# Kernel optimization log

Measured on AMD Instinct MI355X. Metric: run time of the kernel, lower is better.

The kernel has to match this reference:

```python
import jax, jax.numpy as jnp
import numpy as np

B, IN, N, E = 2048, 1024, 64, 128
NEG_SLOPE = 0.01  # torch LeakyReLU default

def setup_inputs() -> dict:
    key = jax.random.key(0)
    k = jax.random.split(key, 5)
    scale_in = 1.0 / np.sqrt(IN)
    scale_ctx = 1.0 / np.sqrt(2 * E)
    return {
        "x": jax.random.normal(k[0], (B, IN), dtype=jnp.float32),
        # stacked per-concept Linear(in_features, 2*emb_size)
        "W_ctx": jax.random.uniform(k[1], (N, IN, 2 * E), jnp.float32, -scale_in, scale_in),
        "b_ctx": jax.random.uniform(k[2], (N, 2 * E), jnp.float32, -scale_in, scale_in),
        # shared Linear(2*emb_size, 1)
        "w_prob": jax.random.uniform(k[3], (2 * E,), jnp.float32, -scale_ctx, scale_ctx),
        "b_prob": jax.random.uniform(k[4], (), jnp.float32, -scale_ctx, scale_ctx),
    }

def reference(x, W_ctx, b_ctx, w_prob, b_prob):
    # context: [B, N, 2E] = LeakyReLU(x @ W_i + b_i) for all concepts i at once
    ctx = jnp.einsum("bi,nio->bno", x, W_ctx) + b_ctx
    ctx = jnp.where(ctx >= 0, ctx, NEG_SLOPE * ctx)
    # shared gate: [B, N]
    c_pred = jax.nn.sigmoid(jnp.einsum("bno,o->bn", ctx, w_prob) + b_prob)
    # gated blend of positive/negative halves -> [B, N, E]
    p = c_pred[..., None]
    c_emb = ctx[..., :E] * p + ctx[..., E:] * (1.0 - p)
    return c_emb, c_pred
```

## Files before the change

kernel.cpp:

```cpp
#include <hip/hip_runtime.h>
#include <hip/hip_bf16.h>

typedef __attribute__((ext_vector_type(8))) short short8v;
typedef __attribute__((ext_vector_type(4))) float floatx4;

#define B_ROWS 2048
#define K_DIM  1024
#define N_CON  64
#define TWO_E  256
#define E_DIM  128
#define BM     128
#define BK     64
#define NT     16
#define LDSA_BYTES (BM * BK * 2)
#define SMEM_BYTES (2 * LDSA_BYTES)
#define EMB_ELEMS 16777216ULL
#define WT_BYTES  33554432ULL
#define XB_BYTES  4194304ULL

static __device__ inline unsigned short bf16bits(float f) {
    __hip_bfloat16 h = __float2bfloat16(f);
    unsigned short u;
    __builtin_memcpy(&u, &h, 2);
    return u;
}

static __device__ inline void dma16(const void* g, void* l) {
    __builtin_amdgcn_global_load_lds(
        (const __attribute__((address_space(1))) unsigned int*)g,
        (__attribute__((address_space(3))) unsigned int*)l,
        16, 0, 0);
}

__global__ void __launch_bounds__(256) prep(const float* __restrict__ W,
                                            const float* __restrict__ x,
                                            unsigned short* __restrict__ Wt,
                                            unsigned short* __restrict__ xb) {
    __shared__ unsigned int lds2[64 * 36];
    const int tid = threadIdx.x;
    const int ot = blockIdx.x, ktile = blockIdx.y, n = blockIdx.z;
    const float* src = W + ((size_t)n * K_DIM + (size_t)ktile * 64) * TWO_E + ot * 64;
    unsigned short* dst = Wt + ((size_t)n * TWO_E + (size_t)ot * 64) * K_DIM + ktile * 64;

    const int kp = tid >> 4;
    const int c  = (tid & 15) * 4;
#pragma unroll
    for (int it = 0; it < 2; ++it) {
        const int k0 = it * 32 + kp * 2;
        floatx4 r0 = *(const floatx4*)&src[(size_t)k0 * TWO_E + c];
        floatx4 r1 = *(const floatx4*)&src[(size_t)(k0 + 1) * TWO_E + c];
#pragma unroll
        for (int j = 0; j < 4; ++j) {
            unsigned int d = (unsigned int)bf16bits(r0[j]) |
                             ((unsigned int)bf16bits(r1[j]) << 16);
            lds2[(c + j) * 36 + it * 16 + kp] = d;
        }
    }
    __syncthreads();
#pragma unroll
    for (int it = 0; it < 2; ++it) {
        int q = it * 256 + tid;
        int o = q >> 3, kc = q & 7;
        short8v v = *(short8v*)&lds2[o * 36 + kc * 4];
        *(short8v*)&dst[(size_t)o * K_DIM + kc * 8] = v;
    }

    const int bid = blockIdx.x + blockIdx.y * 4 + blockIdx.z * 64;
    const size_t base = (size_t)bid * 512 + (size_t)tid * 2;
    unsigned int d = (unsigned int)bf16bits(x[base]) |
                     ((unsigned int)bf16bits(x[base + 1]) << 16);
    ((unsigned int*)xb)[base >> 1] = d;
}

__global__ void __launch_bounds__(256, 2)
concept5(const unsigned short* __restrict__ xb,
         const unsigned short* __restrict__ Wt,
         const float* __restrict__ bc,
         const float* __restrict__ wp,
         const float* __restrict__ bp,
         float* __restrict__ out) {
    __shared__ __align__(16) char smem[SMEM_BYTES];

    const int tid  = threadIdx.x;
    const int wave = tid >> 6;
    const int lane = tid & 63;
    const int lg   = lane >> 4;
    const int l15  = lane & 15;
    const int og   = wave;

    const int lin = blockIdx.y * 16 + blockIdx.x;
    const int nid = (lin & 7) * 128 + (lin >> 3);
    const int rb  = nid & 15;
    const int n   = nid >> 4;

    int otile[4];
#pragma unroll
    for (int oi = 0; oi < 4; ++oi) otile[oi] = og * 32 + (oi & 1) * 16 + (oi & 2) * 64;

    floatx4 acc[8][4];
#pragma unroll
    for (int mi = 0; mi < 8; ++mi)
#pragma unroll
        for (int oi = 0; oi < 4; ++oi) acc[mi][oi] = (floatx4){0.f, 0.f, 0.f, 0.f};

    const unsigned short* xrow = xb + (size_t)rb * BM * K_DIM;
    const unsigned short* wb[4];
#pragma unroll
    for (int oi = 0; oi < 4; ++oi)
        wb[oi] = Wt + ((size_t)n * TWO_E + otile[oi] + l15) * K_DIM + lg * 8;

    const int sw0 = ((lg) ^ (l15 & 7)) * 16;
    const int sw1 = ((4 + lg) ^ (l15 & 7)) * 16;
    const int abase = l15 * 128;

#pragma unroll
    for (int it = 0; it < 4; ++it) {
        int c = it * 4 + wave;
        int s = c * 64 + lane;
        int r = s >> 3, g = s & 7;
        dma16(xrow + (size_t)r * K_DIM + ((g ^ (r & 7)) * 8), smem + c * 1024);
    }
    __syncthreads();

#pragma unroll 1
    for (int t = 0; t < NT; ++t) {
        const int kt = t * BK;
        char* ldsR = smem + (t & 1) * LDSA_BYTES;

        short8v bfr[4][2];
#pragma unroll
        for (int oi = 0; oi < 4; ++oi)
#pragma unroll
            for (int ks = 0; ks < 2; ++ks)
                bfr[oi][ks] = *(const short8v*)(wb[oi] + kt + ks * 32);

        if (t + 1 < NT) {
            char* ldsW = smem + ((t + 1) & 1) * LDSA_BYTES;
            const int ktn = kt + BK;
#pragma unroll
            for (int it = 0; it < 4; ++it) {
                int c = it * 4 + wave;
                int s = c * 64 + lane;
                int r = s >> 3, g = s & 7;
                dma16(xrow + (size_t)r * K_DIM + ktn + ((g ^ (r & 7)) * 8),
                      ldsW + c * 1024);
            }
        }

#pragma unroll
        for (int mi = 0; mi < 8; ++mi) {
            short8v a0 = *(const short8v*)(ldsR + abase + mi * 2048 + sw0);
            short8v a1 = *(const short8v*)(ldsR + abase + mi * 2048 + sw1);
#pragma unroll
            for (int oi = 0; oi < 4; ++oi) {
                acc[mi][oi] = __builtin_amdgcn_mfma_f32_16x16x32_bf16(
                    a0, bfr[oi][0], acc[mi][oi], 0, 0, 0);
                acc[mi][oi] = __builtin_amdgcn_mfma_f32_16x16x32_bf16(
                    a1, bfr[oi][1], acc[mi][oi], 0, 0, 0);
            }
        }

        __syncthreads();
    }

    float biasf[4], wpf[4];
#pragma unroll
    for (int oi = 0; oi < 4; ++oi) {
        int o = otile[oi] + l15;
        biasf[oi] = bc[n * TWO_E + o];
        wpf[oi]  = wp[o];
    }
#pragma unroll
    for (int mi = 0; mi < 8; ++mi)
#pragma unroll
        for (int oi = 0; oi < 4; ++oi)
#pragma unroll
            for (int j = 0; j < 4; ++j) {
                float v = acc[mi][oi][j] + biasf[oi];
                acc[mi][oi][j] = v >= 0.f ? v : 0.01f * v;
            }

    float* partial = (float*)smem;
    float* pv      = (float*)(smem + 2048);

#pragma unroll
    for (int mi = 0; mi < 8; ++mi)
#pragma unroll
        for (int j = 0; j < 4; ++j) {
            float ps = 0.f;
#pragma unroll
            for (int oi = 0; oi < 4; ++oi) ps += acc[mi][oi][j] * wpf[oi];
            ps += __shfl_xor(ps, 1);
            ps += __shfl_xor(ps, 2);
            ps += __shfl_xor(ps, 4);
            ps += __shfl_xor(ps, 8);
            if (l15 == 0) partial[(mi * 16 + lg * 4 + j) * 4 + og] = ps;
        }
    __syncthreads();

    if (tid < 128) {
        float s = partial[tid * 4] + partial[tid * 4 + 1] + partial[tid * 4 + 2] +
                  partial[tid * 4 + 3] + bp[0];
        float p = 1.f / (1.f + __expf(-s));
        pv[tid] = p;
        size_t bi = (size_t)rb * BM + tid;
        out[EMB_ELEMS + bi * N_CON + n] = p;
    }
    __syncthreads();

#pragma unroll
    for (int mi = 0; mi < 8; ++mi)
#pragma unroll
        for (int oi = 0; oi < 2; ++oi)
#pragma unroll
            for (int j = 0; j < 4; ++j) {
                int row = mi * 16 + lg * 4 + j;
                int e = og * 32 + oi * 16 + l15;
                float p = pv[row];
                float v = acc[mi][oi][j] * p + acc[mi][oi + 2][j] * (1.f - p);
                size_t bi = (size_t)rb * BM + row;
                out[(bi * N_CON + n) * E_DIM + e] = v;
            }
}

__global__ void __launch_bounds__(512, 4)
concept_fallback(const float* __restrict__ x,
                 const float* __restrict__ Wc,
                 const float* __restrict__ bc,
                 const float* __restrict__ wp,
                 const float* __restrict__ bp,
                 float* __restrict__ out) {
    __shared__ __align__(16) char smem[49152];
    char* ldsA = smem;
    char* ldsB = smem + 16384;

    const int tid  = threadIdx.x;
    const int wave = tid >> 6;
    const int lane = tid & 63;
    const int lg   = lane >> 4;
    const int l15  = lane & 15;
    const int h    = wave >> 2;
    const int og   = wave & 3;
    const int rb = blockIdx.x;
    const int n  = blockIdx.y;

    int otile[4];
#pragma unroll
    for (int oi = 0; oi < 4; ++oi) otile[oi] = og * 32 + (oi & 1) * 16 + (oi & 2) * 64;

    floatx4 acc[4][4];
#pragma unroll
    for (int mi = 0; mi < 4; ++mi)
#pragma unroll
        for (int oi = 0; oi < 4; ++oi) acc[mi][oi] = (floatx4){0.f, 0.f, 0.f, 0.f};

    const float* xg = x + (size_t)rb * BM * K_DIM;
    const float* wg = Wc + (size_t)n * K_DIM * TWO_E;

    for (int kt = 0; kt < K_DIM; kt += BK) {
#pragma unroll
        for (int it = 0; it < 2; ++it) {
            int s = it * 512 + tid;
            int r = s >> 3, g = s & 7;
            const float* p = xg + (size_t)r * K_DIM + kt + ((g ^ (r & 7)) * 8);
            floatx4 v0 = *(const floatx4*)p, v1 = *(const floatx4*)(p + 4);
            short8v b;
            b[0] = (short)bf16bits(v0[0]); b[1] = (short)bf16bits(v0[1]);
            b[2] = (short)bf16bits(v0[2]); b[3] = (short)bf16bits(v0[3]);
            b[4] = (short)bf16bits(v1[0]); b[5] = (short)bf16bits(v1[1]);
            b[6] = (short)bf16bits(v1[2]); b[7] = (short)bf16bits(v1[3]);
            *(short8v*)(ldsA + s * 16) = b;
        }
#pragma unroll
        for (int it = 0; it < 4; ++it) {
            int s = it * 512 + tid;
            int r = s >> 3, g = s & 7;
            int k0 = kt + (g ^ (r & 7)) * 8;
            short8v b;
#pragma unroll
            for (int j = 0; j < 8; ++j)
                b[j] = (short)bf16bits(wg[(size_t)(k0 + j) * TWO_E + r]);
            *(short8v*)(ldsB + s * 16) = b;
        }
        __syncthreads();

#pragma unroll
        for (int ks = 0; ks < 2; ++ks) {
            const int sw = ((ks * 4 + lg) ^ (l15 & 7)) * 16;
            short8v af[4], bfr[4];
#pragma unroll
            for (int mi = 0; mi < 4; ++mi)
                af[mi] = *(const short8v*)(ldsA + (h * 64 + mi * 16 + l15) * 128 + sw);
#pragma unroll
            for (int oi = 0; oi < 4; ++oi)
                bfr[oi] = *(const short8v*)(ldsB + (otile[oi] + l15) * 128 + sw);
#pragma unroll
            for (int mi = 0; mi < 4; ++mi)
#pragma unroll
                for (int oi = 0; oi < 4; ++oi)
                    acc[mi][oi] = __builtin_amdgcn_mfma_f32_16x16x32_bf16(
                        af[mi], bfr[oi], acc[mi][oi], 0, 0, 0);
        }
        __syncthreads();
    }

    float biasf[4], wpf[4];
#pragma unroll
    for (int oi = 0; oi < 4; ++oi) {
        int o = otile[oi] + l15;
        biasf[oi] = bc[n * TWO_E + o];
        wpf[oi]  = wp[o];
    }
#pragma unroll
    for (int mi = 0; mi < 4; ++mi)
#pragma unroll
        for (int oi = 0; oi < 4; ++oi)
#pragma unroll
            for (int j = 0; j < 4; ++j) {
                float v = acc[mi][oi][j] + biasf[oi];
                acc[mi][oi][j] = v >= 0.f ? v : 0.01f * v;
            }

    float* partial = (float*)smem;
    float* pv      = (float*)(smem + 2048);

#pragma unroll
    for (int mi = 0; mi < 4; ++mi)
#pragma unroll
        for (int j = 0; j < 4; ++j) {
            float ps = 0.f;
#pragma unroll
            for (int oi = 0; oi < 4; ++oi) ps += acc[mi][oi][j] * wpf[oi];
            ps += __shfl_xor(ps, 1);
            ps += __shfl_xor(ps, 2);
            ps += __shfl_xor(ps, 4);
            ps += __shfl_xor(ps, 8);
            if (l15 == 0) partial[(h * 64 + mi * 16 + lg * 4 + j) * 4 + og] = ps;
        }
    __syncthreads();

    if (tid < 128) {
        float s = partial[tid * 4] + partial[tid * 4 + 1] + partial[tid * 4 + 2] +
                  partial[tid * 4 + 3] + bp[0];
        float p = 1.f / (1.f + __expf(-s));
        pv[tid] = p;
        size_t bi = (size_t)rb * BM + tid;
        out[EMB_ELEMS + bi * N_CON + n] = p;
    }
    __syncthreads();

#pragma unroll
    for (int mi = 0; mi < 4; ++mi)
#pragma unroll
        for (int oi = 0; oi < 2; ++oi)
#pragma unroll
            for (int j = 0; j < 4; ++j) {
                int row = h * 64 + mi * 16 + lg * 4 + j;
                int e = og * 32 + oi * 16 + l15;
                float p = pv[row];
                float v = acc[mi][oi][j] * p + acc[mi][oi + 2][j] * (1.f - p);
                size_t bi = (size_t)rb * BM + row;
                out[(bi * N_CON + n) * E_DIM + e] = v;
            }
}

extern "C" void kernel_launch(void* const* d_in, const int* in_sizes, int n_in,
                              void* d_out, int out_size, void* d_ws, size_t ws_size,
                              hipStream_t stream) {
    const float* x  = (const float*)d_in[0];
    const float* Wc = (const float*)d_in[1];
    const float* bc = (const float*)d_in[2];
    const float* wp = (const float*)d_in[3];
    const float* bp = (const float*)d_in[4];
    float* out = (float*)d_out;

    if (ws_size >= WT_BYTES + XB_BYTES) {
        unsigned short* Wt = (unsigned short*)d_ws;
        unsigned short* xb = (unsigned short*)((char*)d_ws + WT_BYTES);
        prep<<<dim3(4, 16, 64), 256, 0, stream>>>(Wc, x, Wt, xb);
        concept5<<<dim3(16, 64), 256, 0, stream>>>(xb, Wt, bc, wp, bp, out);
    } else {
        concept_fallback<<<dim3(16, 64), 512, 0, stream>>>(
            x, Wc, bc, wp, bp, out);
    }
}
```

Before: 212.4 us.

## Prefetch weight fragments one K-tile ahead and shrink prep LDS padding

The main GEMM loop now loads the next K-tile's weight fragments from global memory into a second register buffer while the current tile's MFMAs run. The loop is unrolled by two so the two buffers swap roles without copies, which hides global load latency behind compute. The cost is more live vector registers under a 2-blocks-per-SM launch bound, so spilling is possible. Separately, the prep transpose's LDS row stride drops from 36 to 33 words to change bank mapping, which leaves the 16-byte LDS reads unaligned on odd rows.

```diff
diff --git a/kernel.cpp b/kernel.cpp
--- a/kernel.cpp
+++ b/kernel.cpp
@@ -36,7 +36,7 @@
                                             const float* __restrict__ x,
                                             unsigned short* __restrict__ Wt,
                                             unsigned short* __restrict__ xb) {
-    __shared__ unsigned int lds2[64 * 36];
+    __shared__ unsigned int lds2[64 * 33];
     const int tid = threadIdx.x;
     const int ot = blockIdx.x, ktile = blockIdx.y, n = blockIdx.z;
     const float* src = W + ((size_t)n * K_DIM + (size_t)ktile * 64) * TWO_E + ot * 64;
@@ -53,7 +53,7 @@
         for (int j = 0; j < 4; ++j) {
             unsigned int d = (unsigned int)bf16bits(r0[j]) |
                              ((unsigned int)bf16bits(r1[j]) << 16);
-            lds2[(c + j) * 36 + it * 16 + kp] = d;
+            lds2[(c + j) * 33 + it * 16 + kp] = d;
         }
     }
     __syncthreads();
@@ -61,7 +61,7 @@
     for (int it = 0; it < 2; ++it) {
         int q = it * 256 + tid;
         int o = q >> 3, kc = q & 7;
-        short8v v = *(short8v*)&lds2[o * 36 + kc * 4];
+        short8v v = *(short8v*)&lds2[o * 33 + kc * 4];
         *(short8v*)&dst[(size_t)o * K_DIM + kc * 8] = v;
     }
 
@@ -73,7 +73,7 @@
 }
 
 __global__ void __launch_bounds__(256, 2)
-concept5(const unsigned short* __restrict__ xb,
+concept6(const unsigned short* __restrict__ xb,
          const unsigned short* __restrict__ Wt,
          const float* __restrict__ bc,
          const float* __restrict__ wp,
@@ -120,48 +120,56 @@
         int r = s >> 3, g = s & 7;
         dma16(xrow + (size_t)r * K_DIM + ((g ^ (r & 7)) * 8), smem + c * 1024);
     }
-    __syncthreads();
+    short8v bA[4][2], bB[4][2];
+#pragma unroll
+    for (int oi = 0; oi < 4; ++oi)
+#pragma unroll
+        for (int ks = 0; ks < 2; ++ks)
+            bA[oi][ks] = *(const short8v*)(wb[oi] + ks * 32);
+    __syncthreads();
+
+#define TILE_BODY(T, CUR, NXT)                                                \
+    {                                                                         \
+        const int t_ = (T);                                                   \
+        if (t_ + 1 < NT) {                                                    \
+            const int ktn = (t_ + 1) * BK;                                    \
+            _Pragma("unroll")                                                 \
+            for (int oi = 0; oi < 4; ++oi) {                                  \
+                NXT[oi][0] = *(const short8v*)(wb[oi] + ktn);                  \
+                NXT[oi][1] = *(const short8v*)(wb[oi] + ktn + 32);             \
+            }                                                                 \
+            char* ldsW = smem + ((t_ + 1) & 1) * LDSA_BYTES;                  \
+            _Pragma("unroll")                                                 \
+            for (int it = 0; it < 4; ++it) {                                  \
+                int c = it * 4 + wave;                                        \
+                int s = c * 64 + lane;                                        \
+                int r = s >> 3, g = s & 7;                                    \
+                dma16(xrow + (size_t)r * K_DIM + ktn + ((g ^ (r & 7)) * 8),   \
+                      ldsW + c * 1024);                                       \
+            }                                                                 \
+        }                                                                     \
+        char* ldsR = smem + (t_ & 1) * LDSA_BYTES;                            \
+        _Pragma("unroll")                                                     \
+        for (int mi = 0; mi < 8; ++mi) {                                      \
+            short8v a0 = *(const short8v*)(ldsR + abase + mi * 2048 + sw0);   \
+            short8v a1 = *(const short8v*)(ldsR + abase + mi * 2048 + sw1);   \
+            _Pragma("unroll")                                                 \
+            for (int oi = 0; oi < 4; ++oi) {                                  \
+                acc[mi][oi] = __builtin_amdgcn_mfma_f32_16x16x32_bf16(        \
+                    a0, CUR[oi][0], acc[mi][oi], 0, 0, 0);                    \
+                acc[mi][oi] = __builtin_amdgcn_mfma_f32_16x16x32_bf16(        \
+                    a1, CUR[oi][1], acc[mi][oi], 0, 0, 0);                    \
+            }                                                                 \
+        }                                                                     \
+        __syncthreads();                                                      \
+    }
 
 #pragma unroll 1
-    for (int t = 0; t < NT; ++t) {
-        const int kt = t * BK;
-        char* ldsR = smem + (t & 1) * LDSA_BYTES;
-
-        short8v bfr[4][2];
-#pragma unroll
-        for (int oi = 0; oi < 4; ++oi)
-#pragma unroll
-            for (int ks = 0; ks < 2; ++ks)
-                bfr[oi][ks] = *(const short8v*)(wb[oi] + kt + ks * 32);
-
-        if (t + 1 < NT) {
-            char* ldsW = smem + ((t + 1) & 1) * LDSA_BYTES;
-            const int ktn = kt + BK;
-#pragma unroll
-            for (int it = 0; it < 4; ++it) {
-                int c = it * 4 + wave;
-                int s = c * 64 + lane;
-                int r = s >> 3, g = s & 7;
-                dma16(xrow + (size_t)r * K_DIM + ktn + ((g ^ (r & 7)) * 8),
-                      ldsW + c * 1024);
-            }
-        }
-
-#pragma unroll
-        for (int mi = 0; mi < 8; ++mi) {
-            short8v a0 = *(const short8v*)(ldsR + abase + mi * 2048 + sw0);
-            short8v a1 = *(const short8v*)(ldsR + abase + mi * 2048 + sw1);
-#pragma unroll
-            for (int oi = 0; oi < 4; ++oi) {
-                acc[mi][oi] = __builtin_amdgcn_mfma_f32_16x16x32_bf16(
-                    a0, bfr[oi][0], acc[mi][oi], 0, 0, 0);
-                acc[mi][oi] = __builtin_amdgcn_mfma_f32_16x16x32_bf16(
-                    a1, bfr[oi][1], acc[mi][oi], 0, 0, 0);
-            }
-        }
-
-        __syncthreads();
-    }
+    for (int tp = 0; tp < NT / 2; ++tp) {
+        TILE_BODY(tp * 2,     bA, bB)
+        TILE_BODY(tp * 2 + 1, bB, bA)
+    }
+#undef TILE_BODY
 
     float biasf[4], wpf[4];
 #pragma unroll
@@ -378,7 +386,7 @@
         unsigned short* Wt = (unsigned short*)d_ws;
         unsigned short* xb = (unsigned short*)((char*)d_ws + WT_BYTES);
         prep<<<dim3(4, 16, 64), 256, 0, stream>>>(Wc, x, Wt, xb);
-        concept5<<<dim3(16, 64), 256, 0, stream>>>(xb, Wt, bc, wp, bp, out);
+        concept6<<<dim3(16, 64), 256, 0, stream>>>(xb, Wt, bc, wp, bp, out);
     } else {
         concept_fallback<<<dim3(16, 64), 512, 0, stream>>>(
             x, Wc, bc, wp, bp, out);
```

Result: no change. 211.0 us (-0.7%).
